# Performance work log

Hardware: AMD Instinct MI355X
Metric: run time of the kernel (lower is better)

## Reference

```python
import jax, jax.numpy as jnp
import numpy as np
from jax import lax

KS = 3      # generated depthwise kernel size
F = 9       # utils.FILTERS (channels)
P = 24      # utils.PSZ (patch size); conv stride 8 -> KS = P/8


def _extract_patches(x, p):
    # TF extract_patches with sizes=strides=p, VALID: (B,H,W,C) -> (B,nh,nw,p*p*C)
    B, H, W, C = x.shape
    nh, nw = H // p, W // p
    return (x.reshape(B, nh, p, nw, p, C)
             .transpose(0, 1, 3, 2, 4, 5)
             .reshape(B, nh, nw, p * p * C))


def setup_inputs() -> dict:
    key = jax.random.key(0)
    ks = jax.random.split(key, 6)
    B, H, Wd = 16, 384, 384
    return {
        "guidance": jax.random.normal(ks[0], (B, H, Wd, F), jnp.float32),
        "depth": jax.random.normal(ks[1], (B, H, Wd, F), jnp.float32),
        "conv_w": jax.random.normal(ks[2], (KS, KS, F, 9), jnp.float32) * 0.05,
        "conv_b": jax.random.normal(ks[3], (9,), jnp.float32) * 0.05,
        "dense_w": jax.random.normal(ks[4], (F, F * F), jnp.float32) * 0.05,
        "dense_b": jax.random.normal(ks[5], (F * F,), jnp.float32) * 0.05,
    }


def _forward(guidance, depth, conv_w, conv_b, dense_w, dense_b):
    B, H, W, _ = guidance.shape
    NP = (H // P) * (W // P)
    NB = NP * B
    # raw TF reshape (B,nh,nw,P*P*F) -> (NP,B,P,P,F), reproduced faithfully
    gp = _extract_patches(guidance, P).reshape(NP, B, P, P, F)
    dp = _extract_patches(depth, P).reshape(NP, B, P, P, F)

    # --- KGL: per-patch kernel generation (vectorized over NP*B) ---
    gflat = gp.reshape(NB, P, P, F)
    c = lax.conv_general_dilated(gflat, conv_w, (8, 8), 'SAME',
                                 dimension_numbers=('NHWC', 'HWIO', 'NHWC')) + conv_b
    W_G1 = c.reshape(NP, B, KS, KS, F, 1)
    n1 = jnp.sqrt(jnp.sum(W_G1 * W_G1, axis=(2, 3), keepdims=True))
    W_G1 = W_G1 / jnp.maximum(n1, 1.0)          # tf.clip_by_norm(.., 1, axes=[1,2])

    gap = gp.mean(axis=(2, 3))                   # (NP,B,F)
    d = gap @ dense_w + dense_b                  # (NP,B,F*F)
    W_G2 = d.reshape(NP, B, 1, 1, F, F)
    n2 = jnp.sqrt(jnp.sum(W_G2 * W_G2, axis=(2, 3, 4), keepdims=True))
    W_G2 = W_G2 / jnp.maximum(n2, 1.0)           # clip_by_norm axes=[1,2,3]

    # --- per-sample dynamic depthwise conv (vmap over NP*B) ---
    dw_rhs = W_G1.reshape(NB, KS, KS, F, 1).transpose(0, 1, 2, 4, 3)  # HWIO, groups=F
    dflat = dp.reshape(NB, P, P, F)

    def dwconv(img, f):
        return lax.conv_general_dilated(img[None], f, (1, 1), 'SAME',
                                        dimension_numbers=('NHWC', 'HWIO', 'NHWC'),
                                        feature_group_count=F)[0]

    dc = jax.vmap(dwconv)(dflat, dw_rhs)         # (NB,P,P,F)

    # --- per-sample dynamic 1x1 cross-channel conv == matmul ---
    cc = jnp.einsum('npqi,nio->npqo', dc, W_G2.reshape(NB, F, F))
    # raw TF reshape (NP,B,P,P,F) -> (B,H,W,F), reproduced faithfully
    return cc.reshape(B, H, W, F)


def reference(guidance, depth, conv_w, conv_b, dense_w, dense_b):
    return _forward(guidance, depth, conv_w, conv_b, dense_w, dense_b)
```

## Files before the change

### kernel.cpp

```cpp
#include <hip/hip_runtime.h>
#include <stdint.h>


#define SBAR() __builtin_amdgcn_sched_barrier(0)
#define LGKM0_BAR() \
    asm volatile("s_waitcnt lgkmcnt(0)\n\ts_barrier" ::: "memory")
#define VMCNT9_BAR() \
    asm volatile("s_waitcnt vmcnt(9) lgkmcnt(0)\n\ts_barrier" ::: "memory")

__device__ __forceinline__ void gload16(const float* gsrc, float* ldst) {
    __builtin_amdgcn_global_load_lds(
        (__attribute__((address_space(1))) void*)gsrc,
        (__attribute__((address_space(3))) void*)ldst, 16, 0, 0);
}

__global__ __launch_bounds__(576, 6) void fused_kernel(
    const float* __restrict__ g,
    const float* __restrict__ dep,
    const float* __restrict__ cw,
    const float* __restrict__ cb,
    const float* __restrict__ dw,
    const float* __restrict__ db,
    float* __restrict__ out)
{
    __shared__ __align__(16) float sg[5184];
    __shared__ __align__(16) float sd[5184];
    __shared__ __align__(16) float cwf[729];
    __shared__ __align__(16) float dwf[729];
    __shared__ float cbf[9];
    __shared__ float dbf[81];
    __shared__ float cols[216];
    __shared__ float gapm[9];
    __shared__ float cful[81];
    __shared__ __align__(16) float sw[216];

    const int m = blockIdx.x;
    const int t = threadIdx.x;
    const int b0 = m >> 8, pi = (m >> 4) & 15, pj = m & 15;
    const long rowbase = ((long)(b0 * 384 + pi * 24)) * 3456 + (long)pj * 216;

    for (int idx = t; idx < 729; idx += 576) { cwf[idx] = cw[idx]; dwf[idx] = dw[idx]; }
    if (t < 9) cbf[t] = cb[t];
    if (t >= 64 && t < 145) dbf[t - 64] = db[t - 64];
    SBAR();

    for (int task = t; task < 1296; task += 576) {
        int r = task / 54, c4 = task - r * 54;
        gload16(g + rowbase + (long)r * 3456 + c4 * 4, sg + task * 4);
    }
    SBAR();

    float dn[9];
    #pragma unroll
    for (int k = 0; k < 9; ++k) {
        const int idx = t + 576 * k;
        const int r = idx / 216;
        dn[k] = dep[rowbase + idx + (long)r * 3240];
    }
    SBAR();

    VMCNT9_BAR();

    if (t < 216) {
        float s = 0.f;
        #pragma unroll
        for (int r = 0; r < 24; ++r) s += sg[r * 216 + t];
        cols[t] = s;
    } else if (t >= 256 && t < 337) {
        const int q = t - 256;
        const int o = q % 9, uv = q / 9, v = uv % 3, u = uv / 3;
        float acc = cbf[o];
        #pragma unroll
        for (int du = 0; du < 3; ++du)
        #pragma unroll
        for (int dv = 0; dv < 3; ++dv) {
            const float* gp2 = &sg[(u * 8 + du) * 216 + (v * 8 + dv) * 9];
            const float* wp  = &cwf[(du * 3 + dv) * 81 + o];
            #pragma unroll
            for (int ci = 0; ci < 9; ++ci) acc += gp2[ci] * wp[ci * 9];
        }
        cful[q] = acc;
    }
    LGKM0_BAR();

    if (t < 9) {
        float s = 0.f;
        #pragma unroll
        for (int c = 0; c < 24; ++c) s += cols[c * 9 + t];
        gapm[t] = s * (1.0f / 576.0f);
    } else if (t >= 64 && t < 73) {
        const int f = t - 64;
        float s = 0.f;
        #pragma unroll
        for (int k = 0; k < 9; ++k) { float c = cful[k * 9 + f]; s += c * c; }
        const float scale = (s > 1.0f) ? (1.0f / sqrtf(s)) : 1.0f;
        #pragma unroll
        for (int k = 0; k < 9; ++k) sw[k * 12 + f] = cful[k * 9 + f] * scale;
    }
    LGKM0_BAR();

    #pragma unroll
    for (int k = 0; k < 9; ++k) sd[t + 576 * k] = dn[k];
    if (t < 9) {
        float gv[9];
        #pragma unroll
        for (int k = 0; k < 9; ++k) gv[k] = gapm[k];
        float d[9];
        float s = 0.f;
        #pragma unroll
        for (int i = 0; i < 9; ++i) {
            float a = dbf[i * 9 + t];
            #pragma unroll
            for (int k = 0; k < 9; ++k) a += gv[k] * dwf[k * 81 + i * 9 + t];
            d[i] = a; s += a * a;
        }
        const float scale = (s > 1.0f) ? (1.0f / sqrtf(s)) : 1.0f;
        #pragma unroll
        for (int i = 0; i < 9; ++i) sw[108 + t * 12 + i] = d[i] * scale;
    }
    LGKM0_BAR();

    {
        const int row = t / 24;
        const int col = t - row * 24;
        float dc[9];
        #pragma unroll
        for (int i = 0; i < 9; ++i) dc[i] = 0.f;

        #pragma unroll
        for (int du = 0; du < 3; ++du) {
            const int r = row + du - 1;
            if (r < 0 || r > 23) continue;
            #pragma unroll
            for (int dv = 0; dv < 3; ++dv) {
                const int c = col + dv - 1;
                if (c < 0 || c > 23) continue;
                const float* sp = &sd[r * 216 + c * 9];
                const float* wv = &sw[(du * 3 + dv) * 12];
                #pragma unroll
                for (int i = 0; i < 9; ++i) dc[i] += sp[i] * wv[i];
            }
        }

        float* op = out + (long)m * 5184 + t * 9;
        #pragma unroll
        for (int o = 0; o < 9; ++o) {
            const float* wv = &sw[108 + o * 12];
            float a = 0.f;
            #pragma unroll
            for (int i = 0; i < 9; ++i) a += dc[i] * wv[i];
            op[o] = a;
        }
    }
}

extern "C" void kernel_launch(void* const* d_in, const int* in_sizes, int n_in,
                              void* d_out, int out_size, void* d_ws, size_t ws_size,
                              hipStream_t stream) {
    const float* g  = (const float*)d_in[0];
    const float* dp = (const float*)d_in[1];
    const float* cw = (const float*)d_in[2];
    const float* cb = (const float*)d_in[3];
    const float* dw = (const float*)d_in[4];
    const float* db = (const float*)d_in[5];
    float* out = (float*)d_out;
    (void)d_ws; (void)ws_size;

    fused_kernel<<<dim3(4096), dim3(576), 0, stream>>>(g, dp, cw, cb, dw, db, out);
}
```

Measured before the change: 227.9 us.

## Alias guidance and depth LDS buffers, pad depth pixels, broadcast weights via readlane

```diff
diff --git a/kernel.cpp b/kernel.cpp
--- a/kernel.cpp
+++ b/kernel.cpp
@@ -14,6 +14,10 @@
         (__attribute__((address_space(3))) void*)ldst, 16, 0, 0);
 }
 
+__device__ __forceinline__ float rlane(float v, int l) {
+    return __int_as_float(__builtin_amdgcn_readlane(__float_as_int(v), l));
+}
+
 __global__ __launch_bounds__(576, 6) void fused_kernel(
     const float* __restrict__ g,
     const float* __restrict__ dep,
@@ -23,8 +27,7 @@
     const float* __restrict__ db,
     float* __restrict__ out)
 {
-    __shared__ __align__(16) float sg[5184];
-    __shared__ __align__(16) float sd[5184];
+    __shared__ __align__(16) float s_gd[6912];
     __shared__ __align__(16) float cwf[729];
     __shared__ __align__(16) float dwf[729];
     __shared__ float cbf[9];
@@ -32,7 +35,7 @@
     __shared__ float cols[216];
     __shared__ float gapm[9];
     __shared__ float cful[81];
-    __shared__ __align__(16) float sw[216];
+    __shared__ __align__(16) float sw[256];
 
     const int m = blockIdx.x;
     const int t = threadIdx.x;
@@ -46,7 +49,7 @@
 
     for (int task = t; task < 1296; task += 576) {
         int r = task / 54, c4 = task - r * 54;
-        gload16(g + rowbase + (long)r * 3456 + c4 * 4, sg + task * 4);
+        gload16(g + rowbase + (long)r * 3456 + c4 * 4, s_gd + task * 4);
     }
     SBAR();
 
@@ -64,7 +67,7 @@
     if (t < 216) {
         float s = 0.f;
         #pragma unroll
-        for (int r = 0; r < 24; ++r) s += sg[r * 216 + t];
+        for (int r = 0; r < 24; ++r) s += s_gd[r * 216 + t];
         cols[t] = s;
     } else if (t >= 256 && t < 337) {
         const int q = t - 256;
@@ -74,7 +77,7 @@
         for (int du = 0; du < 3; ++du)
         #pragma unroll
         for (int dv = 0; dv < 3; ++dv) {
-            const float* gp2 = &sg[(u * 8 + du) * 216 + (v * 8 + dv) * 9];
+            const float* gp2 = &s_gd[(u * 8 + du) * 216 + (v * 8 + dv) * 9];
             const float* wp  = &cwf[(du * 3 + dv) * 81 + o];
             #pragma unroll
             for (int ci = 0; ci < 9; ++ci) acc += gp2[ci] * wp[ci * 9];
@@ -95,12 +98,16 @@
         for (int k = 0; k < 9; ++k) { float c = cful[k * 9 + f]; s += c * c; }
         const float scale = (s > 1.0f) ? (1.0f / sqrtf(s)) : 1.0f;
         #pragma unroll
-        for (int k = 0; k < 9; ++k) sw[k * 12 + f] = cful[k * 9 + f] * scale;
+        for (int k = 0; k < 9; ++k) sw[k * 9 + f] = cful[k * 9 + f] * scale;
     }
     LGKM0_BAR();
 
     #pragma unroll
-    for (int k = 0; k < 9; ++k) sd[t + 576 * k] = dn[k];
+    for (int k = 0; k < 9; ++k) {
+        const int idx = t + 576 * k;
+        const int pix = idx / 9, ch = idx - pix * 9;
+        s_gd[pix * 12 + ch] = dn[k];
+    }
     if (t < 9) {
         float gv[9];
         #pragma unroll
@@ -116,11 +123,17 @@
         }
         const float scale = (s > 1.0f) ? (1.0f / sqrtf(s)) : 1.0f;
         #pragma unroll
-        for (int i = 0; i < 9; ++i) sw[108 + t * 12 + i] = d[i] * scale;
+        for (int i = 0; i < 9; ++i) sw[96 + t * 9 + i] = d[i] * scale;
     }
     LGKM0_BAR();
 
     {
+        const int l = t & 63;
+        const float a1 = sw[l];
+        const float a2 = sw[64 + l];
+        const float b1 = sw[96 + l];
+        const float b2 = sw[160 + l];
+
         const int row = t / 24;
         const int col = t - row * 24;
         float dc[9];
@@ -135,20 +148,31 @@
             for (int dv = 0; dv < 3; ++dv) {
                 const int c = col + dv - 1;
                 if (c < 0 || c > 23) continue;
-                const float* sp = &sd[r * 216 + c * 9];
-                const float* wv = &sw[(du * 3 + dv) * 12];
+                const float* sp = &s_gd[(r * 24 + c) * 12];
+                const float4 A = *reinterpret_cast<const float4*>(sp);
+                const float4 B = *reinterpret_cast<const float4*>(sp + 4);
+                const float a8 = sp[8];
+                const int tap = du * 3 + dv;
+                const float v[9] = { A.x, A.y, A.z, A.w, B.x, B.y, B.z, B.w, a8 };
                 #pragma unroll
-                for (int i = 0; i < 9; ++i) dc[i] += sp[i] * wv[i];
+                for (int i = 0; i < 9; ++i) {
+                    const int wi = tap * 9 + i;
+                    const float w = (wi < 64) ? rlane(a1, wi) : rlane(a2, wi - 64);
+                    dc[i] += v[i] * w;
+                }
             }
         }
 
         float* op = out + (long)m * 5184 + t * 9;
         #pragma unroll
         for (int o = 0; o < 9; ++o) {
-            const float* wv = &sw[108 + o * 12];
             float a = 0.f;
             #pragma unroll
-            for (int i = 0; i < 9; ++i) a += dc[i] * wv[i];
+            for (int i = 0; i < 9; ++i) {
+                const int wi = o * 9 + i;
+                const float w = (wi < 64) ? rlane(b1, wi) : rlane(b2, wi - 64);
+                a += dc[i] * w;
+            }
             op[o] = a;
         }
     }
```

Result: no change. 226.0 us (-0.9%).
